# Performance work log

Hardware: AMD Instinct MI355X
Metric: run time of the kernel (lower is better)

## Reference

```python
import jax, jax.numpy as jnp
import numpy as np

NUM_CLASSES = 256
WEIGHT = 0.0005
EPS = 1e-12  # torch F.normalize eps


def setup_inputs() -> dict:
    key = jax.random.key(0)
    k1, k2 = jax.random.split(key)
    features = jax.random.normal(k1, (32768, 1024), dtype=jnp.float32)
    labels = jax.random.randint(k2, (32768,), 0, NUM_CLASSES, dtype=jnp.int32)
    return {"features": features, "labels": labels}


def _centroid_loss(features, labels):
    B, D = features.shape
    # row-wise L2 normalize (torch F.normalize: x / max(||x||, eps))
    norms = jnp.linalg.norm(features, axis=1, keepdims=True)
    f = features / jnp.maximum(norms, EPS)

    ones = jnp.ones((B,), f.dtype)
    counts = jax.ops.segment_sum(ones, labels, num_segments=NUM_CLASSES)  # [C]
    sums = jax.ops.segment_sum(f, labels, num_segments=NUM_CLASSES)       # [C, D]

    # rank of each sample within its class (order of first appearance),
    # matching the row order of features[class_mask] in the original loop
    onehot = jax.nn.one_hot(labels, NUM_CLASSES, dtype=jnp.int32)          # [B, C]
    rank = jnp.take_along_axis(jnp.cumsum(onehot, axis=0), labels[:, None].astype(jnp.int32), axis=1)[:, 0] - 1

    # idx_table[c, r] = global index of the r-th member of class c; sentinel B if none
    idx_table = jnp.full((NUM_CLASSES, B), B, dtype=jnp.int32)
    idx_table = idx_table.at[labels, rank].set(jnp.arange(B, dtype=jnp.int32))

    # NOTE: the original code indexes class_features with the GLOBAL index i
    # (arange(n_c) != i), i.e. it excludes the member of the class at position i,
    # and excludes nothing when i >= n_c. We reproduce that exactly.
    arange_b = jnp.arange(B)
    k = idx_table[labels, arange_b]            # class member at in-class position i (global i)
    valid_excl = k < B                          # exclusion only happens when i < class size
    excl_feat = jnp.where(valid_excl[:, None], f[jnp.where(valid_excl, k, 0)], 0.0)

    n_c = counts[labels]                        # class size per sample (float)
    denom = jnp.where(valid_excl, n_c - 1.0, n_c)
    denom = jnp.maximum(denom, 1.0)             # safe for masked-out singleton classes
    centroid = (sums[labels] - excl_feat) / denom[:, None]

    dist = jnp.mean((f - centroid) ** 2, axis=1)  # F.mse_loss(..., reduction='mean')
    contrib = jnp.where(n_c > 1.0, dist, 0.0)     # skip classes with <=1 sample
    return WEIGHT * jnp.sum(contrib) / B


def reference(features, labels):
    return _centroid_loss(features, labels)
```

## Files before the change

### kernel.cpp

```cpp
#include <hip/hip_runtime.h>

#define BN 32768
#define DN 1024
#define CN 256
#define RCAP 512

__device__ __forceinline__ float dot4(float4 a, float4 b) {
    return a.x*b.x + a.y*b.y + a.z*b.z + a.w*b.w;
}

__global__ void __launch_bounds__(1024) k_main(const float4* __restrict__ x4,
                                               const int* __restrict__ labels,
                                               int* __restrict__ idx,
                                               int* __restrict__ counts,
                                               float* __restrict__ rnorm,
                                               float* __restrict__ sums,
                                               float* __restrict__ snorm2,
                                               float* __restrict__ acc) {
    __shared__ unsigned int packed[BN / 4];
    __shared__ int sic[RCAP];
    __shared__ int wcnt[16];
    __shared__ float facc[(DN / 4) * 5];
    __shared__ float wred[4];

    const int c = blockIdx.x;
    const int t = threadIdx.x;

    for (int w = t; w < BN / 4; w += 1024) {
        const int4 v = ((const int4*)labels)[w];
        packed[w] = (unsigned int)(v.x & 255)
                  | ((unsigned int)(v.y & 255) << 8)
                  | ((unsigned int)(v.z & 255) << 16)
                  | ((unsigned int)(v.w & 255) << 24);
    }
    for (int i = t; i < (DN / 4) * 5; i += 1024) facc[i] = 0.0f;
    __syncthreads();

    const int wave = t >> 6, lane = t & 63;
    const unsigned long long lt = (lane == 0) ? 0ull : (~0ull >> (64 - lane));
    const int ch0 = wave * 32, ch1 = ch0 + 32;

    int cnt = 0;
    for (int ch = ch0; ch < ch1; ++ch) {
        const int gi = ch * 64 + lane;
        const int lab = (packed[gi >> 2] >> ((gi & 3) * 8)) & 255;
        cnt += __popcll(__ballot(lab == c));
    }
    if (lane == 0) wcnt[wave] = cnt;
    __syncthreads();

    int base = 0, ntot = 0;
    for (int w2 = 0; w2 < 16; ++w2) {
        const int v = wcnt[w2];
        if (w2 < wave) base += v;
        ntot += v;
    }

    for (int ch = ch0; ch < ch1; ++ch) {
        const int gi = ch * 64 + lane;
        const int lab = (packed[gi >> 2] >> ((gi & 3) * 8)) & 255;
        const bool pred = (lab == c);
        const unsigned long long mask = __ballot(pred);
        if (pred) {
            const int pos = base + __popcll(mask & lt);
            if (pos < RCAP) { sic[pos] = gi; idx[c * RCAP + pos] = gi; }
        }
        base += __popcll(mask);
    }
    if (t == 0) counts[c] = ntot;
    __syncthreads();

    const int nn = min(ntot, RCAP);
    float4 a0 = make_float4(0.f, 0.f, 0.f, 0.f), a1 = a0, a2 = a0, a3 = a0;
    for (int r = wave; r < nn; r += 16) {
        const int row = sic[r];
        const float4* b4 = x4 + (size_t)row * 256;
        const float4 v0 = b4[lane];
        const float4 v1 = b4[lane + 64];
        const float4 v2 = b4[lane + 128];
        const float4 v3 = b4[lane + 192];
        float ss = dot4(v0, v0) + dot4(v1, v1) + dot4(v2, v2) + dot4(v3, v3);
#pragma unroll
        for (int off = 32; off; off >>= 1) ss += __shfl_xor(ss, off, 64);
        const float rn = 1.0f / fmaxf(sqrtf(ss), 1e-12f);
        if (lane == 0) rnorm[row] = rn;
        a0.x += v0.x * rn; a0.y += v0.y * rn; a0.z += v0.z * rn; a0.w += v0.w * rn;
        a1.x += v1.x * rn; a1.y += v1.y * rn; a1.z += v1.z * rn; a1.w += v1.w * rn;
        a2.x += v2.x * rn; a2.y += v2.y * rn; a2.z += v2.z * rn; a2.w += v2.w * rn;
        a3.x += v3.x * rn; a3.y += v3.y * rn; a3.z += v3.z * rn; a3.w += v3.w * rn;
    }

    {
        const int q0 = lane, q1 = lane + 64, q2 = lane + 128, q3 = lane + 192;
        atomicAdd(&facc[5 * q0 + 0], a0.x); atomicAdd(&facc[5 * q0 + 1], a0.y);
        atomicAdd(&facc[5 * q0 + 2], a0.z); atomicAdd(&facc[5 * q0 + 3], a0.w);
        atomicAdd(&facc[5 * q1 + 0], a1.x); atomicAdd(&facc[5 * q1 + 1], a1.y);
        atomicAdd(&facc[5 * q1 + 2], a1.z); atomicAdd(&facc[5 * q1 + 3], a1.w);
        atomicAdd(&facc[5 * q2 + 0], a2.x); atomicAdd(&facc[5 * q2 + 1], a2.y);
        atomicAdd(&facc[5 * q2 + 2], a2.z); atomicAdd(&facc[5 * q2 + 3], a2.w);
        atomicAdd(&facc[5 * q3 + 0], a3.x); atomicAdd(&facc[5 * q3 + 1], a3.y);
        atomicAdd(&facc[5 * q3 + 2], a3.z); atomicAdd(&facc[5 * q3 + 3], a3.w);
    }
    __syncthreads();

    float d = 0.0f;
    if (t < 256) {
        float4 tot;
        tot.x = facc[5 * t + 0]; tot.y = facc[5 * t + 1];
        tot.z = facc[5 * t + 2]; tot.w = facc[5 * t + 3];
        ((float4*)sums)[(size_t)c * 256 + t] = tot;
        d = dot4(tot, tot);
    }
    if (wave < 4) {
#pragma unroll
        for (int off = 32; off; off >>= 1) d += __shfl_xor(d, off, 64);
        if (lane == 0) wred[wave] = d;
    }
    __syncthreads();
    if (t == 0) {
        const float s2 = wred[0] + wred[1] + wred[2] + wred[3];
        snorm2[c] = s2;
        if (ntot > 1) {
            const float nf = (float)ntot;
            atomicAdd(acc, (nf - s2 / nf) * (1.0f / DN));
        }
    }
}

__global__ void __launch_bounds__(256) k_corr(const float4* __restrict__ x4,
                                              const int* __restrict__ labels,
                                              const int* __restrict__ counts,
                                              const int* __restrict__ idx,
                                              const float* __restrict__ rnorm,
                                              const float* __restrict__ sums,
                                              const float* __restrict__ snorm2,
                                              float* __restrict__ acc) {
    const int i = blockIdx.x;
    const int c = labels[i];
    const int n = counts[c];
    if (i >= n || n < 2 || i >= RCAP) return;
    const int k = idx[c * RCAP + i];
    const int t = threadIdx.x;

    const float4 xi = x4[(size_t)i * 256 + t];
    const float4 xk = x4[(size_t)k * 256 + t];
    const float4 s  = ((const float4*)sums)[(size_t)c * 256 + t];

    float d0 = dot4(xi, s);
    float d1 = dot4(xi, xk);
    float d2 = dot4(xk, s);
    float d3 = dot4(xk, xk);
#pragma unroll
    for (int off = 32; off; off >>= 1) {
        d0 += __shfl_xor(d0, off, 64);
        d1 += __shfl_xor(d1, off, 64);
        d2 += __shfl_xor(d2, off, 64);
        d3 += __shfl_xor(d3, off, 64);
    }
    __shared__ float4 wred[4];
    if ((t & 63) == 0) wred[t >> 6] = make_float4(d0, d1, d2, d3);
    __syncthreads();
    if (t == 0) {
        const float xiS  = wred[0].x + wred[1].x + wred[2].x + wred[3].x;
        const float xixk = wred[0].y + wred[1].y + wred[2].y + wred[3].y;
        const float xkS  = wred[0].z + wred[1].z + wred[2].z + wred[3].z;
        const float xkxk = wred[0].w + wred[1].w + wred[2].w + wred[3].w;
        const float rni = rnorm[i], rnk = rnorm[k], s2 = snorm2[c];
        const float fiS  = rni * xiS;
        const float fifk = rni * rnk * xixk;
        const float Sfk  = rnk * xkS;
        const float fk2  = rnk * rnk * xkxk;
        const float nf = (float)n;
        const float dd = nf - 1.0f;
        const float naive = -2.0f * fiS / nf + s2 / (nf * nf);
        const float corr  = -2.0f * (fiS - fifk) / dd + (s2 - 2.0f * Sfk + fk2) / (dd * dd);
        atomicAdd(acc, (corr - naive) * (1.0f / DN));
    }
}

__global__ void k_fin(const float* __restrict__ acc, float* __restrict__ out) {
    out[0] = (0.0005f / (float)BN) * acc[0];
}

extern "C" void kernel_launch(void* const* d_in, const int* in_sizes, int n_in,
                              void* d_out, int out_size, void* d_ws, size_t ws_size,
                              hipStream_t stream) {
    const float* features = (const float*)d_in[0];
    const int* labels = (const int*)d_in[1];
    float* out = (float*)d_out;

    char* ws = (char*)d_ws;
    float* rnorm  = (float*)(ws + 0);
    float* sums   = (float*)(ws + 131072);
    int*   idx    = (int*)  (ws + 1179648);
    int*   counts = (int*)  (ws + 1703936);
    float* snorm2 = (float*)(ws + 1704960);
    float* acc    = (float*)(ws + 1705984);

    const float4* x4 = (const float4*)features;

    hipMemsetAsync(acc, 0, sizeof(float), stream);
    k_main<<<CN, 1024, 0, stream>>>(x4, labels, idx, counts, rnorm, sums, snorm2, acc);
    k_corr<<<RCAP, 256, 0, stream>>>(x4, labels, counts, idx, rnorm, sums, snorm2, acc);
    k_fin<<<1, 1, 0, stream>>>(acc, out);
}
```

Baseline: 221.9 us.

## Split per-class reduction across row slices and fold correction into per-class finish

```diff
diff --git a/kernel.cpp b/kernel.cpp
--- a/kernel.cpp
+++ b/kernel.cpp
@@ -3,42 +3,48 @@
 #define BN 32768
 #define DN 1024
 #define CN 256
-#define RCAP 512
+#define NSLICE 8
+#define SROWS (BN / NSLICE)
+#define SCAP 56
 
 __device__ __forceinline__ float dot4(float4 a, float4 b) {
     return a.x*b.x + a.y*b.y + a.z*b.z + a.w*b.w;
 }
 
-__global__ void __launch_bounds__(1024) k_main(const float4* __restrict__ x4,
-                                               const int* __restrict__ labels,
-                                               int* __restrict__ idx,
-                                               int* __restrict__ counts,
-                                               float* __restrict__ rnorm,
-                                               float* __restrict__ sums,
-                                               float* __restrict__ snorm2,
-                                               float* __restrict__ acc) {
-    __shared__ unsigned int packed[BN / 4];
-    __shared__ int sic[RCAP];
-    __shared__ int wcnt[16];
-    __shared__ float facc[(DN / 4) * 5];
-    __shared__ float wred[4];
-
-    const int c = blockIdx.x;
+__global__ void __launch_bounds__(256, 8) k_sum(const float4* __restrict__ x4,
+                                                const int* __restrict__ labels,
+                                                float* __restrict__ sums,
+                                                float* __restrict__ rnorm,
+                                                int* __restrict__ idx_part,
+                                                int* __restrict__ cnt_part) {
+    __shared__ unsigned int packed[SROWS / 4];
+    __shared__ int lm[SCAP];
+    __shared__ int wcnt[4];
+    __shared__ float fa[(DN / 4) * 5];
+
+    const int bid = blockIdx.x;
+    const int c = bid >> 3;
+    const int s = bid & 7;
     const int t = threadIdx.x;
-
-    for (int w = t; w < BN / 4; w += 1024) {
-        const int4 v = ((const int4*)labels)[w];
-        packed[w] = (unsigned int)(v.x & 255)
-                  | ((unsigned int)(v.y & 255) << 8)
-                  | ((unsigned int)(v.z & 255) << 16)
-                  | ((unsigned int)(v.w & 255) << 24);
-    }
-    for (int i = t; i < (DN / 4) * 5; i += 1024) facc[i] = 0.0f;
+    const int row0 = s * SROWS;
+
+    {
+        const int4* l4 = (const int4*)labels + s * (SROWS / 16);
+        for (int w = t; w < SROWS / 4; w += 256) {
+            const int4 v = ((const int4*)((const int*)labels + row0))[w];
+            packed[w] = (unsigned int)(v.x & 255)
+                      | ((unsigned int)(v.y & 255) << 8)
+                      | ((unsigned int)(v.z & 255) << 16)
+                      | ((unsigned int)(v.w & 255) << 24);
+        }
+        (void)l4;
+    }
+    for (int i = t; i < (DN / 4) * 5; i += 256) fa[i] = 0.0f;
     __syncthreads();
 
     const int wave = t >> 6, lane = t & 63;
     const unsigned long long lt = (lane == 0) ? 0ull : (~0ull >> (64 - lane));
-    const int ch0 = wave * 32, ch1 = ch0 + 32;
+    const int ch0 = wave * 16, ch1 = ch0 + 16;
 
     int cnt = 0;
     for (int ch = ch0; ch < ch1; ++ch) {
@@ -50,7 +56,7 @@
     __syncthreads();
 
     int base = 0, ntot = 0;
-    for (int w2 = 0; w2 < 16; ++w2) {
+    for (int w2 = 0; w2 < 4; ++w2) {
         const int v = wcnt[w2];
         if (w2 < wave) base += v;
         ntot += v;
@@ -63,17 +69,21 @@
         const unsigned long long mask = __ballot(pred);
         if (pred) {
             const int pos = base + __popcll(mask & lt);
-            if (pos < RCAP) { sic[pos] = gi; idx[c * RCAP + pos] = gi; }
+            if (pos < SCAP) {
+                const int grow = row0 + gi;
+                lm[pos] = grow;
+                idx_part[bid * SCAP + pos] = grow;
+            }
         }
         base += __popcll(mask);
     }
-    if (t == 0) counts[c] = ntot;
-    __syncthreads();
-
-    const int nn = min(ntot, RCAP);
+    if (t == 0) cnt_part[bid] = ntot;
+    __syncthreads();
+
+    const int m = min(ntot, SCAP);
     float4 a0 = make_float4(0.f, 0.f, 0.f, 0.f), a1 = a0, a2 = a0, a3 = a0;
-    for (int r = wave; r < nn; r += 16) {
-        const int row = sic[r];
+    for (int p = wave; p < m; p += 4) {
+        const int row = lm[p];
         const float4* b4 = x4 + (size_t)row * 256;
         const float4 v0 = b4[lane];
         const float4 v1 = b4[lane + 64];
@@ -92,115 +102,135 @@
 
     {
         const int q0 = lane, q1 = lane + 64, q2 = lane + 128, q3 = lane + 192;
-        atomicAdd(&facc[5 * q0 + 0], a0.x); atomicAdd(&facc[5 * q0 + 1], a0.y);
-        atomicAdd(&facc[5 * q0 + 2], a0.z); atomicAdd(&facc[5 * q0 + 3], a0.w);
-        atomicAdd(&facc[5 * q1 + 0], a1.x); atomicAdd(&facc[5 * q1 + 1], a1.y);
-        atomicAdd(&facc[5 * q1 + 2], a1.z); atomicAdd(&facc[5 * q1 + 3], a1.w);
-        atomicAdd(&facc[5 * q2 + 0], a2.x); atomicAdd(&facc[5 * q2 + 1], a2.y);
-        atomicAdd(&facc[5 * q2 + 2], a2.z); atomicAdd(&facc[5 * q2 + 3], a2.w);
-        atomicAdd(&facc[5 * q3 + 0], a3.x); atomicAdd(&facc[5 * q3 + 1], a3.y);
-        atomicAdd(&facc[5 * q3 + 2], a3.z); atomicAdd(&facc[5 * q3 + 3], a3.w);
-    }
-    __syncthreads();
-
-    float d = 0.0f;
-    if (t < 256) {
-        float4 tot;
-        tot.x = facc[5 * t + 0]; tot.y = facc[5 * t + 1];
-        tot.z = facc[5 * t + 2]; tot.w = facc[5 * t + 3];
-        ((float4*)sums)[(size_t)c * 256 + t] = tot;
-        d = dot4(tot, tot);
-    }
-    if (wave < 4) {
+        atomicAdd(&fa[5 * q0 + 0], a0.x); atomicAdd(&fa[5 * q0 + 1], a0.y);
+        atomicAdd(&fa[5 * q0 + 2], a0.z); atomicAdd(&fa[5 * q0 + 3], a0.w);
+        atomicAdd(&fa[5 * q1 + 0], a1.x); atomicAdd(&fa[5 * q1 + 1], a1.y);
+        atomicAdd(&fa[5 * q1 + 2], a1.z); atomicAdd(&fa[5 * q1 + 3], a1.w);
+        atomicAdd(&fa[5 * q2 + 0], a2.x); atomicAdd(&fa[5 * q2 + 1], a2.y);
+        atomicAdd(&fa[5 * q2 + 2], a2.z); atomicAdd(&fa[5 * q2 + 3], a2.w);
+        atomicAdd(&fa[5 * q3 + 0], a3.x); atomicAdd(&fa[5 * q3 + 1], a3.y);
+        atomicAdd(&fa[5 * q3 + 2], a3.z); atomicAdd(&fa[5 * q3 + 3], a3.w);
+    }
+    __syncthreads();
+
+    {
+        float* dst = sums + (size_t)c * DN + 4 * t;
+        atomicAdd(dst + 0, fa[5 * t + 0]);
+        atomicAdd(dst + 1, fa[5 * t + 1]);
+        atomicAdd(dst + 2, fa[5 * t + 2]);
+        atomicAdd(dst + 3, fa[5 * t + 3]);
+    }
+}
+
+__global__ void __launch_bounds__(256) k_finish(const float4* __restrict__ x4,
+                                                const float* __restrict__ sums,
+                                                const float* __restrict__ rnorm,
+                                                const int* __restrict__ idx_part,
+                                                const int* __restrict__ cnt_part,
+                                                float* __restrict__ out) {
+    __shared__ int sic[NSLICE * SCAP];
+    __shared__ int scc[NSLICE], spre[NSLICE], sn, snn;
+    __shared__ float wred[4];
+    __shared__ float4 cred[4];
+
+    const int c = blockIdx.x;
+    const int t = threadIdx.x;
+    const int wave = t >> 6, lane = t & 63;
+
+    if (t == 0) {
+        int n = 0, nn = 0;
+        for (int i2 = 0; i2 < NSLICE; ++i2) {
+            const int cv = cnt_part[c * NSLICE + i2];
+            n += cv;
+            const int cc = min(cv, SCAP);
+            scc[i2] = cc;
+            spre[i2] = nn;
+            nn += cc;
+        }
+        sn = n; snn = nn;
+    }
+    __syncthreads();
+    const int n = sn, nn = snn;
+    if (n < 2) return;
+
+    const float4 Sq = ((const float4*)sums)[(size_t)c * 256 + t];
+
+    float d = dot4(Sq, Sq);
 #pragma unroll
-        for (int off = 32; off; off >>= 1) d += __shfl_xor(d, off, 64);
-        if (lane == 0) wred[wave] = d;
-    }
-    __syncthreads();
+    for (int off = 32; off; off >>= 1) d += __shfl_xor(d, off, 64);
+    if (lane == 0) wred[wave] = d;
+
+    for (int u = t; u < NSLICE * SCAP; u += 256) {
+        const int s2i = u / SCAP;
+        const int r = u - s2i * SCAP;
+        if (r < scc[s2i]) sic[spre[s2i] + r] = idx_part[(c * NSLICE + s2i) * SCAP + r];
+    }
+    __syncthreads();
+
+    const float s2 = wred[0] + wred[1] + wred[2] + wred[3];
+    const int nlim = min(n, nn);
+
+    float dacc = 0.0f;
+    for (int p = 0; p < nn; ++p) {
+        const int j = sic[p];
+        if (j >= nlim) continue;
+        const int k = sic[j];
+        const float4 xi = x4[(size_t)j * 256 + t];
+        const float4 xk = x4[(size_t)k * 256 + t];
+        float d0 = dot4(xi, Sq);
+        float d1 = dot4(xi, xk);
+        float d2 = dot4(xk, Sq);
+        float d3 = dot4(xk, xk);
+#pragma unroll
+        for (int off = 32; off; off >>= 1) {
+            d0 += __shfl_xor(d0, off, 64);
+            d1 += __shfl_xor(d1, off, 64);
+            d2 += __shfl_xor(d2, off, 64);
+            d3 += __shfl_xor(d3, off, 64);
+        }
+        if (lane == 0) cred[wave] = make_float4(d0, d1, d2, d3);
+        __syncthreads();
+        if (t == 0) {
+            const float xiS  = cred[0].x + cred[1].x + cred[2].x + cred[3].x;
+            const float xixk = cred[0].y + cred[1].y + cred[2].y + cred[3].y;
+            const float xkS  = cred[0].z + cred[1].z + cred[2].z + cred[3].z;
+            const float xkxk = cred[0].w + cred[1].w + cred[2].w + cred[3].w;
+            const float rni = rnorm[j], rnk = rnorm[k];
+            const float fiS  = rni * xiS;
+            const float fifk = rni * rnk * xixk;
+            const float Sfk  = rnk * xkS;
+            const float fk2  = rnk * rnk * xkxk;
+            const float nf = (float)n;
+            const float dd = nf - 1.0f;
+            const float naive = -2.0f * fiS / nf + s2 / (nf * nf);
+            const float corr  = -2.0f * (fiS - fifk) / dd + (s2 - 2.0f * Sfk + fk2) / (dd * dd);
+            dacc += corr - naive;
+        }
+        __syncthreads();
+    }
+
     if (t == 0) {
-        const float s2 = wred[0] + wred[1] + wred[2] + wred[3];
-        snorm2[c] = s2;
-        if (ntot > 1) {
-            const float nf = (float)ntot;
-            atomicAdd(acc, (nf - s2 / nf) * (1.0f / DN));
-        }
-    }
-}
-
-__global__ void __launch_bounds__(256) k_corr(const float4* __restrict__ x4,
-                                              const int* __restrict__ labels,
-                                              const int* __restrict__ counts,
-                                              const int* __restrict__ idx,
-                                              const float* __restrict__ rnorm,
-                                              const float* __restrict__ sums,
-                                              const float* __restrict__ snorm2,
-                                              float* __restrict__ acc) {
-    const int i = blockIdx.x;
-    const int c = labels[i];
-    const int n = counts[c];
-    if (i >= n || n < 2 || i >= RCAP) return;
-    const int k = idx[c * RCAP + i];
-    const int t = threadIdx.x;
-
-    const float4 xi = x4[(size_t)i * 256 + t];
-    const float4 xk = x4[(size_t)k * 256 + t];
-    const float4 s  = ((const float4*)sums)[(size_t)c * 256 + t];
-
-    float d0 = dot4(xi, s);
-    float d1 = dot4(xi, xk);
-    float d2 = dot4(xk, s);
-    float d3 = dot4(xk, xk);
-#pragma unroll
-    for (int off = 32; off; off >>= 1) {
-        d0 += __shfl_xor(d0, off, 64);
-        d1 += __shfl_xor(d1, off, 64);
-        d2 += __shfl_xor(d2, off, 64);
-        d3 += __shfl_xor(d3, off, 64);
-    }
-    __shared__ float4 wred[4];
-    if ((t & 63) == 0) wred[t >> 6] = make_float4(d0, d1, d2, d3);
-    __syncthreads();
-    if (t == 0) {
-        const float xiS  = wred[0].x + wred[1].x + wred[2].x + wred[3].x;
-        const float xixk = wred[0].y + wred[1].y + wred[2].y + wred[3].y;
-        const float xkS  = wred[0].z + wred[1].z + wred[2].z + wred[3].z;
-        const float xkxk = wred[0].w + wred[1].w + wred[2].w + wred[3].w;
-        const float rni = rnorm[i], rnk = rnorm[k], s2 = snorm2[c];
-        const float fiS  = rni * xiS;
-        const float fifk = rni * rnk * xixk;
-        const float Sfk  = rnk * xkS;
-        const float fk2  = rnk * rnk * xkxk;
         const float nf = (float)n;
-        const float dd = nf - 1.0f;
-        const float naive = -2.0f * fiS / nf + s2 / (nf * nf);
-        const float corr  = -2.0f * (fiS - fifk) / dd + (s2 - 2.0f * Sfk + fk2) / (dd * dd);
-        atomicAdd(acc, (corr - naive) * (1.0f / DN));
-    }
-}
-
-__global__ void k_fin(const float* __restrict__ acc, float* __restrict__ out) {
-    out[0] = (0.0005f / (float)BN) * acc[0];
+        const float total = (nf - s2 / nf) + dacc;
+        atomicAdd(out, total * (1.0f / DN) * (0.0005f / (float)BN));
+    }
 }
 
 extern "C" void kernel_launch(void* const* d_in, const int* in_sizes, int n_in,
                               void* d_out, int out_size, void* d_ws, size_t ws_size,
                               hipStream_t stream) {
-    const float* features = (const float*)d_in[0];
+    const float4* x4 = (const float4*)d_in[0];
     const int* labels = (const int*)d_in[1];
     float* out = (float*)d_out;
 
     char* ws = (char*)d_ws;
-    float* rnorm  = (float*)(ws + 0);
-    float* sums   = (float*)(ws + 131072);
-    int*   idx    = (int*)  (ws + 1179648);
-    int*   counts = (int*)  (ws + 1703936);
-    float* snorm2 = (float*)(ws + 1704960);
-    float* acc    = (float*)(ws + 1705984);
-
-    const float4* x4 = (const float4*)features;
-
-    hipMemsetAsync(acc, 0, sizeof(float), stream);
-    k_main<<<CN, 1024, 0, stream>>>(x4, labels, idx, counts, rnorm, sums, snorm2, acc);
-    k_corr<<<RCAP, 256, 0, stream>>>(x4, labels, counts, idx, rnorm, sums, snorm2, acc);
-    k_fin<<<1, 1, 0, stream>>>(acc, out);
-}
+    float* sums     = (float*)(ws + 0);
+    float* rnorm    = (float*)(ws + 1048576);
+    int*   idx_part = (int*)  (ws + 1179648);
+    int*   cnt_part = (int*)  (ws + 1638400);
+
+    hipMemsetAsync(sums, 0, (size_t)CN * DN * sizeof(float), stream);
+    hipMemsetAsync(out, 0, sizeof(float), stream);
+    k_sum<<<CN * NSLICE, 256, 0, stream>>>(x4, labels, sums, rnorm, idx_part, cnt_part);
+    k_finish<<<CN, 256, 0, stream>>>(x4, sums, rnorm, idx_part, cnt_part, out);
+}
```

Result: slower. 236.2 us (+6.4%).
